# Optimization experiments

Hardware: AMD Instinct MI355X
Metric: run time of the kernel (lower is better)

## Reference

```python
import jax, jax.numpy as jnp
import numpy as np

NUM_HEADS = 12


def setup_inputs() -> dict:
    key = jax.random.key(0)
    ks = jax.random.split(key, 20)
    T, B, D = 1024, 8, 768
    s = 1.0 / np.sqrt(D)
    inp = {
        "query": jax.random.normal(ks[0], (T, B, D), jnp.float32),
        "key": jax.random.normal(ks[1], (T, B, D), jnp.float32),
        "value": jax.random.normal(ks[2], (T, B, D), jnp.float32),
        "ls_len": 512,
    }
    names = ["Wq", "Wk", "Wv", "Wqm", "Wkm", "Wvm", "Wo"]
    for i, n in enumerate(names):
        inp[n] = jax.random.normal(ks[3 + i], (D, D), jnp.float32) * s
        inp["b" + n[1:]] = jnp.zeros((D,), jnp.float32)
    return inp


def reference(query, key, value, ls_len, Wq, bq, Wk, bk, Wv, bv,
              Wqm, bqm, Wkm, bkm, Wvm, bvm, Wo, bo):
    T, B, D = query.shape
    H = NUM_HEADS
    hd = D // H
    scaling = float(hd) ** -0.5

    def proj(x, W, b):
        return x @ W.T + b

    # modal-split projections along the sequence (dim 0), then re-concat
    q = jnp.concatenate([proj(query[:ls_len], Wq, bq),
                         proj(query[ls_len:], Wqm, bqm)], axis=0) * scaling
    k = jnp.concatenate([proj(key[:ls_len], Wk, bk),
                         proj(key[ls_len:], Wkm, bkm)], axis=0)
    v = jnp.concatenate([proj(value[:ls_len], Wv, bv),
                         proj(value[ls_len:], Wvm, bvm)], axis=0)

    # (T, B, D) -> (B*H, T, hd)
    def to_heads(x):
        return x.reshape(x.shape[0], B * H, hd).transpose(1, 0, 2)

    q, k, v = to_heads(q), to_heads(k), to_heads(v)
    scores = jnp.einsum("bth,bsh->bts", q, k)        # (B*H, T, S)
    attn = jax.nn.softmax(scores, axis=-1)
    out = jnp.einsum("bts,bsh->bth", attn, v)        # (B*H, T, hd)
    out = out.transpose(1, 0, 2).reshape(T, B, D)
    return out @ Wo.T + bo
```

## Files before the change

kernel.cpp:

```cpp
#include <hip/hip_runtime.h>

#define T_  1024
#define B_  8
#define D_  768
#define H_  12
#define HD_ 64
#define BH_ 96
#define M_  8192
#define XSZ 6291456ull
#define WSZ 589824ull

typedef __attribute__((ext_vector_type(8))) short short8;
typedef __attribute__((ext_vector_type(4))) float f32x4;

__device__ __forceinline__ unsigned short f2bf(float f) {
    unsigned int u = __float_as_uint(f);
    u += 0x7FFF + ((u >> 16) & 1);
    return (unsigned short)(u >> 16);
}

__device__ __forceinline__ void g2lds16(const unsigned short* g, unsigned short* l) {
    __builtin_amdgcn_global_load_lds(
        (const __attribute__((address_space(1))) unsigned int*)(g),
        (__attribute__((address_space(3))) unsigned int*)(l),
        16, 0, 0);
}

__global__ __launch_bounds__(256)
void convert_kernel(const float* __restrict__ q, const float* __restrict__ k,
                    const float* __restrict__ v,
                    const float* __restrict__ wq, const float* __restrict__ wk,
                    const float* __restrict__ wv, const float* __restrict__ wqm,
                    const float* __restrict__ wkm, const float* __restrict__ wvm,
                    const float* __restrict__ wo,
                    unsigned short* __restrict__ dst)
{
    const int seg = blockIdx.y;
    const float* s; size_t off, n;
    switch (seg) {
        case 0: s = q;   off = 0;               n = XSZ; break;
        case 1: s = k;   off = XSZ;             n = XSZ; break;
        case 2: s = v;   off = 2*XSZ;           n = XSZ; break;
        case 3: s = wq;  off = 3*XSZ;           n = WSZ; break;
        case 4: s = wk;  off = 3*XSZ +   WSZ;   n = WSZ; break;
        case 5: s = wv;  off = 3*XSZ + 2*WSZ;   n = WSZ; break;
        case 6: s = wqm; off = 3*XSZ + 3*WSZ;   n = WSZ; break;
        case 7: s = wkm; off = 3*XSZ + 4*WSZ;   n = WSZ; break;
        case 8: s = wvm; off = 3*XSZ + 5*WSZ;   n = WSZ; break;
        default:s = wo;  off = 3*XSZ + 6*WSZ;   n = WSZ; break;
    }
    unsigned short* d = dst + off;
    const size_t stride = (size_t)gridDim.x * blockDim.x;
    for (size_t i = (size_t)blockIdx.x * blockDim.x + threadIdx.x; i < n / 4; i += stride) {
        const float4 f = reinterpret_cast<const float4*>(s)[i];
        ushort4 o;
        o.x = f2bf(f.x); o.y = f2bf(f.y); o.z = f2bf(f.z); o.w = f2bf(f.w);
        reinterpret_cast<ushort4*>(d)[i] = o;
    }
}

__device__ __forceinline__ void stage_tile32(const unsigned short* __restrict__ A,
                                             const unsigned short* __restrict__ B,
                                             int m0, int n0, int ks,
                                             unsigned short* lds, int buf, int tid)
{
    const int w = tid >> 6, l = tid & 63;
    const int rsub = l >> 2;
    const int cg   = (l & 3) ^ ((l >> 3) & 3);
    const int koff = ks * 32 + cg * 8;
    #pragma unroll
    for (int p = 0; p < 2; ++p) {
        const int rbase = p * 64 + w * 16;
        const int row   = rbase + rsub;
        g2lds16(&A[(size_t)(m0 + row) * D_ + koff],
                &lds[buf * 8192 + rbase * 32]);
        g2lds16(&B[(size_t)(n0 + row) * D_ + koff],
                &lds[buf * 8192 + 4096 + rbase * 32]);
    }
}

__device__ __forceinline__ void mfma_step32(const unsigned short* lds, int buf,
                                            int wr, int wc, int lr, int lg,
                                            f32x4 acc[4][4])
{
    const int slot = (lg ^ ((lr >> 1) & 3)) * 8;
    short8 a[4], b[4];
    #pragma unroll
    for (int m = 0; m < 4; ++m)
        a[m] = *reinterpret_cast<const short8*>(
            &lds[buf * 8192 + (wr * 64 + 16 * m + lr) * 32 + slot]);
    #pragma unroll
    for (int n = 0; n < 4; ++n)
        b[n] = *reinterpret_cast<const short8*>(
            &lds[buf * 8192 + 4096 + (wc * 64 + 16 * n + lr) * 32 + slot]);
    #pragma unroll
    for (int m = 0; m < 4; ++m)
        #pragma unroll
        for (int n = 0; n < 4; ++n)
            acc[m][n] = __builtin_amdgcn_mfma_f32_16x16x32_bf16(a[m], b[n], acc[m][n], 0, 0, 0);
}

#define GEMM_CORE(Aptr, Bptr)                                                  \
    f32x4 acc[4][4];                                                           \
    _Pragma("unroll") for (int m = 0; m < 4; ++m)                              \
        _Pragma("unroll") for (int n = 0; n < 4; ++n)                          \
            acc[m][n] = (f32x4){0.f, 0.f, 0.f, 0.f};                           \
    stage_tile32(Aptr, Bptr, m0, n0, 0, lds, 0, tid);                          \
    asm volatile("s_waitcnt vmcnt(0)" ::: "memory");                           \
    __builtin_amdgcn_s_barrier();                                              \
    for (int ks = 0; ks < 24; ++ks) {                                          \
        __builtin_amdgcn_sched_barrier(0);                                     \
        if (ks < 23) stage_tile32(Aptr, Bptr, m0, n0, ks + 1, lds, (ks + 1) & 1, tid); \
        mfma_step32(lds, ks & 1, wr, wc, lr, lg, acc);                         \
        asm volatile("s_waitcnt vmcnt(0) lgkmcnt(0)" ::: "memory");            \
        __builtin_amdgcn_sched_barrier(0);                                     \
        __builtin_amdgcn_s_barrier();                                          \
        __builtin_amdgcn_sched_barrier(0);                                     \
    }

__global__ __launch_bounds__(256)
void qkv_gemm(const unsigned short* __restrict__ xb,
              const unsigned short* __restrict__ wb,
              const int* __restrict__ ls_ptr,
              const float* __restrict__ bq,  const float* __restrict__ bk,
              const float* __restrict__ bv,  const float* __restrict__ bqm,
              const float* __restrict__ bkm, const float* __restrict__ bvm,
              unsigned short* __restrict__ qh, unsigned short* __restrict__ kh,
              unsigned short* __restrict__ vt)
{
    __shared__ unsigned short lds[16384];
    const int bid = blockIdx.x;
    const int L   = (bid & 7) * 144 + (bid >> 3);
    const int z   = L / 384;
    const int rem = L - z * 384;
    const int mi  = rem / 6;
    const int ni  = rem - mi * 6;
    const int m0 = mi * 128, n0 = ni * 128;

    const int tid = threadIdx.x;
    const int w = tid >> 6, l = tid & 63, lr = l & 15, lg = l >> 4;
    const int wr = w >> 1, wc = w & 1;

    const bool modal = (m0 >= ls_ptr[0] * B_);
    const unsigned short* A = xb + (size_t)z * XSZ;
    const unsigned short* W = wb + (size_t)(z + (modal ? 3 : 0)) * WSZ;
    const float* bias = modal ? (z == 0 ? bqm : z == 1 ? bkm : bvm)
                              : (z == 0 ? bq  : z == 1 ? bk  : bv);

    GEMM_CORE(A, W)

    float bn[4];
    #pragma unroll
    for (int n = 0; n < 4; ++n) bn[n] = bias[n0 + wc * 64 + 16 * n + lr];

    if (z < 2) {
        unsigned short* dst = (z == 0) ? qh : kh;
        const float scale = (z == 0) ? 0.18033688011112042f : 1.0f;
        #pragma unroll
        for (int m = 0; m < 4; ++m) {
            const int grb = m0 + wr * 64 + 16 * m + 4 * lg;
            #pragma unroll
            for (int n = 0; n < 4; ++n) {
                const int gc = n0 + wc * 64 + 16 * n + lr;
                const int h = gc >> 6, e = gc & 63;
                #pragma unroll
                for (int j = 0; j < 4; ++j) {
                    const int gr = grb + j, t = gr >> 3, b = gr & 7;
                    dst[((size_t)(b * H_ + h) * T_ + t) * HD_ + e] =
                        f2bf((acc[m][n][j] + bn[n]) * scale);
                }
            }
        }
    } else {
        #pragma unroll
        for (int m = 0; m < 4; ++m) {
            const int grb = m0 + wr * 64 + 16 * m + 4 * lg;
            #pragma unroll
            for (int n = 0; n < 4; ++n) {
                const int gc = n0 + wc * 64 + 16 * n + lr;
                const int h = gc >> 6, e = gc & 63;
                #pragma unroll
                for (int j = 0; j < 4; ++j) {
                    const int gr = grb + j, t = gr >> 3, b = gr & 7;
                    vt[((size_t)(b * H_ + h) * HD_ + e) * T_ + t] =
                        f2bf(acc[m][n][j] + bn[n]);
                }
            }
        }
    }
}

__global__ __launch_bounds__(256)
void out_gemm(const unsigned short* __restrict__ aob,
              const unsigned short* __restrict__ wo,
              const float* __restrict__ bo, float* __restrict__ out)
{
    __shared__ unsigned short lds[16384];
    const int bid = blockIdx.x;
    const int L   = (bid & 7) * 48 + (bid >> 3);
    const int mi  = L / 6, ni = L - mi * 6;
    const int m0 = mi * 128, n0 = ni * 128;

    const int tid = threadIdx.x;
    const int w = tid >> 6, l = tid & 63, lr = l & 15, lg = l >> 4;
    const int wr = w >> 1, wc = w & 1;

    GEMM_CORE(aob, wo)

    float bn[4];
    #pragma unroll
    for (int n = 0; n < 4; ++n) bn[n] = bo[n0 + wc * 64 + 16 * n + lr];

    #pragma unroll
    for (int m = 0; m < 4; ++m) {
        const int grb = m0 + wr * 64 + 16 * m + 4 * lg;
        #pragma unroll
        for (int n = 0; n < 4; ++n) {
            const int gc = n0 + wc * 64 + 16 * n + lr;
            #pragma unroll
            for (int j = 0; j < 4; ++j) {
                const int gr = grb + j;
                out[(size_t)gr * D_ + gc] = acc[m][n][j] + bn[n];
            }
        }
    }
}

__device__ __forceinline__ void stage_kv(const unsigned short* __restrict__ khh,
                                         const unsigned short* __restrict__ vth,
                                         int kt, unsigned short* KsB,
                                         unsigned short* VtB, int w, int l)
{
    const int rbase = w * 8;
    const int row   = rbase + (l >> 3);
    const int cg    = (l & 7) ^ ((l >> 3) & 7);
    g2lds16(&khh[(size_t)(kt * 64 + row) * HD_ + cg * 8], &KsB[rbase * 64]);
    g2lds16(&vth[(size_t)row * T_ + kt * 64 + cg * 8],    &VtB[rbase * 64]);
}

__global__ __launch_bounds__(512)
void attn_kernel_bf16(const unsigned short* __restrict__ qh,
                      const unsigned short* __restrict__ kh,
                      const unsigned short* __restrict__ vt,
                      unsigned short* __restrict__ aob)
{
    const int bid = blockIdx.x;
    const int L   = (bid & 7) * 96 + (bid >> 3);
    const int bh  = L >> 3;
    const int qt  = L & 7;

    const int tid = threadIdx.x;
    const int w   = tid >> 6;
    const int l   = tid & 63;
    const int lr  = l & 15;
    const int lg  = l >> 4;

    __shared__ unsigned short Ks[2][4096];
    __shared__ unsigned short Vt[2][4096];
    __shared__ unsigned short Ps[8192];

    const unsigned short* khh = kh + (size_t)bh * T_ * HD_;
    const unsigned short* vth = vt + (size_t)bh * HD_ * T_;
    const size_t qk_head = (size_t)bh * T_ * HD_;

    short8 qf[2];
    #pragma unroll
    for (int c = 0; c < 2; ++c)
        qf[c] = *reinterpret_cast<const short8*>(
            &qh[qk_head + (size_t)(qt * 128 + 16 * w + lr) * HD_ + 8 * lg + 32 * c]);

    const short one_bf = (short)0x3F80;
    const short8 ones8 = {one_bf, one_bf, one_bf, one_bf,
                          one_bf, one_bf, one_bf, one_bf};

    f32x4 o[4];
    #pragma unroll
    for (int ef = 0; ef < 4; ++ef) o[ef] = (f32x4){0.f, 0.f, 0.f, 0.f};
    f32x4 lsumf = (f32x4){0.f, 0.f, 0.f, 0.f};

    stage_kv(khh, vth, 0, Ks[0], Vt[0], w, l);
    asm volatile("s_waitcnt vmcnt(0)" ::: "memory");
    __builtin_amdgcn_s_barrier();

    int buf = 0;
    for (int kt = 0; kt < 16; ++kt) {
        __builtin_amdgcn_sched_barrier(0);
        if (kt < 15)
            stage_kv(khh, vth, kt + 1, Ks[buf ^ 1], Vt[buf ^ 1], w, l);

        f32x4 s[4];
        #pragma unroll
        for (int nf = 0; nf < 4; ++nf) s[nf] = (f32x4){0.f, 0.f, 0.f, 0.f};
        #pragma unroll
        for (int c = 0; c < 2; ++c) {
            #pragma unroll
            for (int nf = 0; nf < 4; ++nf) {
                const short8 kb = *reinterpret_cast<const short8*>(
                    &Ks[buf][(16 * nf + lr) * 64 + ((8 * lg + 32 * c) ^ ((lr & 7) << 3))]);
                s[nf] = __builtin_amdgcn_mfma_f32_16x16x32_bf16(qf[c], kb, s[nf], 0, 0, 0);
            }
        }

        #pragma unroll
        for (int r = 0; r < 4; ++r) {
            const int q  = 16 * w + 4 * lg + r;
            const int qx = ((4 * lg + r) & 7) << 3;
            #pragma unroll
            for (int nf = 0; nf < 4; ++nf)
                Ps[q * 64 + ((16 * nf + lr) ^ qx)] =
                    f2bf(exp2f(s[nf][r] - 16.0f));
        }
        asm volatile("s_waitcnt lgkmcnt(0)" ::: "memory");
        __builtin_amdgcn_sched_barrier(0);
        __builtin_amdgcn_s_barrier();
        __builtin_amdgcn_sched_barrier(0);

        const int prow = 16 * w + lr;
        #pragma unroll
        for (int c = 0; c < 2; ++c) {
            const short8 pa = *reinterpret_cast<const short8*>(
                &Ps[prow * 64 + ((8 * lg + 32 * c) ^ ((prow & 7) << 3))]);
            #pragma unroll
            for (int ef = 0; ef < 4; ++ef) {
                const short8 vb = *reinterpret_cast<const short8*>(
                    &Vt[buf][(16 * ef + lr) * 64 + ((8 * lg + 32 * c) ^ ((lr & 7) << 3))]);
                o[ef] = __builtin_amdgcn_mfma_f32_16x16x32_bf16(pa, vb, o[ef], 0, 0, 0);
            }
            lsumf = __builtin_amdgcn_mfma_f32_16x16x32_bf16(pa, ones8, lsumf, 0, 0, 0);
        }

        asm volatile("s_waitcnt vmcnt(0) lgkmcnt(0)" ::: "memory");
        __builtin_amdgcn_sched_barrier(0);
        __builtin_amdgcn_s_barrier();
        __builtin_amdgcn_sched_barrier(0);
        buf ^= 1;
    }

    const int b = bh / H_, h = bh % H_;
    #pragma unroll
    for (int r = 0; r < 4; ++r) {
        const int t = qt * 128 + 16 * w + 4 * lg + r;
        const float inv = 1.0f / lsumf[r];
        #pragma unroll
        for (int ef = 0; ef < 4; ++ef)
            aob[((size_t)t * B_ + b) * D_ + h * HD_ + 16 * ef + lr] =
                f2bf(o[ef][r] * inv);
    }
}

extern "C" void kernel_launch(void* const* d_in, const int* in_sizes, int n_in,
                              void* d_out, int out_size, void* d_ws, size_t ws_size,
                              hipStream_t stream)
{
    const float* query = (const float*)d_in[0];
    const float* keyi  = (const float*)d_in[1];
    const float* value = (const float*)d_in[2];
    const int*   lsp   = (const int*)  d_in[3];
    const float* Wq  = (const float*)d_in[4],  *bq  = (const float*)d_in[5];
    const float* Wk  = (const float*)d_in[6],  *bk  = (const float*)d_in[7];
    const float* Wv  = (const float*)d_in[8],  *bv  = (const float*)d_in[9];
    const float* Wqm = (const float*)d_in[10], *bqm = (const float*)d_in[11];
    const float* Wkm = (const float*)d_in[12], *bkm = (const float*)d_in[13];
    const float* Wvm = (const float*)d_in[14], *bvm = (const float*)d_in[15];
    const float* Wo  = (const float*)d_in[16], *bo  = (const float*)d_in[17];

    unsigned short* ws = (unsigned short*)d_ws;
    unsigned short* xb  = ws;
    unsigned short* wb  = xb + 3 * XSZ;
    unsigned short* qh  = wb + 7 * WSZ;
    unsigned short* kh  = qh + XSZ;
    unsigned short* vt  = kh + XSZ;
    unsigned short* aob = vt + XSZ;

    dim3 gc_(512, 10);
    convert_kernel<<<gc_, 256, 0, stream>>>(query, keyi, value,
                                            Wq, Wk, Wv, Wqm, Wkm, Wvm, Wo, xb);

    qkv_gemm<<<1152, 256, 0, stream>>>(xb, wb, lsp, bq, bk, bv, bqm, bkm, bvm,
                                       qh, kh, vt);

    attn_kernel_bf16<<<768, 512, 0, stream>>>(qh, kh, vt, aob);

    out_gemm<<<384, 256, 0, stream>>>(aob, wb + 6 * WSZ, bo, (float*)d_out);
}
```

Baseline: 187.4 us.

## Fuse fp32-to-bf16 activation conversion into QKV GEMM and triple-buffer out GEMM

```diff
diff --git a/kernel.cpp b/kernel.cpp
--- a/kernel.cpp
+++ b/kernel.cpp
@@ -27,31 +27,26 @@
 }
 
 __global__ __launch_bounds__(256)
-void convert_kernel(const float* __restrict__ q, const float* __restrict__ k,
-                    const float* __restrict__ v,
-                    const float* __restrict__ wq, const float* __restrict__ wk,
-                    const float* __restrict__ wv, const float* __restrict__ wqm,
-                    const float* __restrict__ wkm, const float* __restrict__ wvm,
-                    const float* __restrict__ wo,
-                    unsigned short* __restrict__ dst)
+void convert_w_kernel(const float* __restrict__ wq, const float* __restrict__ wk,
+                      const float* __restrict__ wv, const float* __restrict__ wqm,
+                      const float* __restrict__ wkm, const float* __restrict__ wvm,
+                      const float* __restrict__ wo,
+                      unsigned short* __restrict__ dst)
 {
     const int seg = blockIdx.y;
-    const float* s; size_t off, n;
+    const float* s;
     switch (seg) {
-        case 0: s = q;   off = 0;               n = XSZ; break;
-        case 1: s = k;   off = XSZ;             n = XSZ; break;
-        case 2: s = v;   off = 2*XSZ;           n = XSZ; break;
-        case 3: s = wq;  off = 3*XSZ;           n = WSZ; break;
-        case 4: s = wk;  off = 3*XSZ +   WSZ;   n = WSZ; break;
-        case 5: s = wv;  off = 3*XSZ + 2*WSZ;   n = WSZ; break;
-        case 6: s = wqm; off = 3*XSZ + 3*WSZ;   n = WSZ; break;
-        case 7: s = wkm; off = 3*XSZ + 4*WSZ;   n = WSZ; break;
-        case 8: s = wvm; off = 3*XSZ + 5*WSZ;   n = WSZ; break;
-        default:s = wo;  off = 3*XSZ + 6*WSZ;   n = WSZ; break;
-    }
-    unsigned short* d = dst + off;
+        case 0: s = wq;  break;
+        case 1: s = wk;  break;
+        case 2: s = wv;  break;
+        case 3: s = wqm; break;
+        case 4: s = wkm; break;
+        case 5: s = wvm; break;
+        default:s = wo;  break;
+    }
+    unsigned short* d = dst + (size_t)seg * WSZ;
     const size_t stride = (size_t)gridDim.x * blockDim.x;
-    for (size_t i = (size_t)blockIdx.x * blockDim.x + threadIdx.x; i < n / 4; i += stride) {
+    for (size_t i = (size_t)blockIdx.x * blockDim.x + threadIdx.x; i < WSZ / 4; i += stride) {
         const float4 f = reinterpret_cast<const float4*>(s)[i];
         ushort4 o;
         o.x = f2bf(f.x); o.y = f2bf(f.y); o.z = f2bf(f.z); o.w = f2bf(f.w);
@@ -59,26 +54,6 @@
     }
 }
 
-__device__ __forceinline__ void stage_tile32(const unsigned short* __restrict__ A,
-                                             const unsigned short* __restrict__ B,
-                                             int m0, int n0, int ks,
-                                             unsigned short* lds, int buf, int tid)
-{
-    const int w = tid >> 6, l = tid & 63;
-    const int rsub = l >> 2;
-    const int cg   = (l & 3) ^ ((l >> 3) & 3);
-    const int koff = ks * 32 + cg * 8;
-    #pragma unroll
-    for (int p = 0; p < 2; ++p) {
-        const int rbase = p * 64 + w * 16;
-        const int row   = rbase + rsub;
-        g2lds16(&A[(size_t)(m0 + row) * D_ + koff],
-                &lds[buf * 8192 + rbase * 32]);
-        g2lds16(&B[(size_t)(n0 + row) * D_ + koff],
-                &lds[buf * 8192 + 4096 + rbase * 32]);
-    }
-}
-
 __device__ __forceinline__ void mfma_step32(const unsigned short* lds, int buf,
                                             int wr, int wc, int lr, int lg,
                                             f32x4 acc[4][4])
@@ -100,26 +75,10 @@
             acc[m][n] = __builtin_amdgcn_mfma_f32_16x16x32_bf16(a[m], b[n], acc[m][n], 0, 0, 0);
 }
 
-#define GEMM_CORE(Aptr, Bptr)                                                  \
-    f32x4 acc[4][4];                                                           \
-    _Pragma("unroll") for (int m = 0; m < 4; ++m)                              \
-        _Pragma("unroll") for (int n = 0; n < 4; ++n)                          \
-            acc[m][n] = (f32x4){0.f, 0.f, 0.f, 0.f};                           \
-    stage_tile32(Aptr, Bptr, m0, n0, 0, lds, 0, tid);                          \
-    asm volatile("s_waitcnt vmcnt(0)" ::: "memory");                           \
-    __builtin_amdgcn_s_barrier();                                              \
-    for (int ks = 0; ks < 24; ++ks) {                                          \
-        __builtin_amdgcn_sched_barrier(0);                                     \
-        if (ks < 23) stage_tile32(Aptr, Bptr, m0, n0, ks + 1, lds, (ks + 1) & 1, tid); \
-        mfma_step32(lds, ks & 1, wr, wc, lr, lg, acc);                         \
-        asm volatile("s_waitcnt vmcnt(0) lgkmcnt(0)" ::: "memory");            \
-        __builtin_amdgcn_sched_barrier(0);                                     \
-        __builtin_amdgcn_s_barrier();                                          \
-        __builtin_amdgcn_sched_barrier(0);                                     \
-    }
-
 __global__ __launch_bounds__(256)
-void qkv_gemm(const unsigned short* __restrict__ xb,
+void qkv_gemm(const float* __restrict__ query,
+              const float* __restrict__ keyi,
+              const float* __restrict__ value,
               const unsigned short* __restrict__ wb,
               const int* __restrict__ ls_ptr,
               const float* __restrict__ bq,  const float* __restrict__ bk,
@@ -142,12 +101,76 @@
     const int wr = w >> 1, wc = w & 1;
 
     const bool modal = (m0 >= ls_ptr[0] * B_);
-    const unsigned short* A = xb + (size_t)z * XSZ;
+    const float* A32 = (z == 0) ? query : (z == 1) ? keyi : value;
     const unsigned short* W = wb + (size_t)(z + (modal ? 3 : 0)) * WSZ;
     const float* bias = modal ? (z == 0 ? bqm : z == 1 ? bkm : bvm)
                               : (z == 0 ? bq  : z == 1 ? bk  : bv);
 
-    GEMM_CORE(A, W)
+    const int arow_s = tid >> 2;
+    const int ac     = tid & 3;
+    const int aslot  = (ac ^ ((tid >> 3) & 3)) * 8;
+
+    float4 ax[2][2];
+
+#define LOADX(ks)                                                              \
+    _Pragma("unroll") for (int p = 0; p < 2; ++p) {                            \
+        const float* src = &A32[(size_t)(m0 + p * 64 + arow_s) * D_ +          \
+                                (ks) * 32 + ac * 8];                           \
+        ax[p][0] = *reinterpret_cast<const float4*>(src);                      \
+        ax[p][1] = *reinterpret_cast<const float4*>(src + 4);                  \
+    }
+
+#define WRITEX(buf)                                                            \
+    _Pragma("unroll") for (int p = 0; p < 2; ++p) {                            \
+        unsigned short v8[8];                                                  \
+        v8[0] = f2bf(ax[p][0].x); v8[1] = f2bf(ax[p][0].y);                    \
+        v8[2] = f2bf(ax[p][0].z); v8[3] = f2bf(ax[p][0].w);                    \
+        v8[4] = f2bf(ax[p][1].x); v8[5] = f2bf(ax[p][1].y);                    \
+        v8[6] = f2bf(ax[p][1].z); v8[7] = f2bf(ax[p][1].w);                    \
+        *reinterpret_cast<short8*>(                                            \
+            &lds[(buf) * 8192 + (p * 64 + arow_s) * 32 + aslot]) =             \
+            *reinterpret_cast<const short8*>(v8);                              \
+    }
+
+#define STAGEB(ks, buf)                                                        \
+    {                                                                          \
+        const int rsub = l >> 2;                                               \
+        const int cg   = (l & 3) ^ ((l >> 3) & 3);                             \
+        const int koff = (ks) * 32 + cg * 8;                                   \
+        _Pragma("unroll") for (int p = 0; p < 2; ++p) {                        \
+            const int rbase = p * 64 + w * 16;                                 \
+            g2lds16(&W[(size_t)(n0 + rbase + rsub) * D_ + koff],               \
+                    &lds[(buf) * 8192 + 4096 + rbase * 32]);                   \
+        }                                                                      \
+    }
+
+    f32x4 acc[4][4];
+    #pragma unroll
+    for (int m = 0; m < 4; ++m)
+        #pragma unroll
+        for (int n = 0; n < 4; ++n)
+            acc[m][n] = (f32x4){0.f, 0.f, 0.f, 0.f};
+
+    LOADX(0)
+    STAGEB(0, 0)
+    WRITEX(0)
+    __syncthreads();
+
+    int buf = 0;
+    for (int ks = 0; ks < 24; ++ks) {
+        if (ks < 23) {
+            LOADX(ks + 1)
+            STAGEB(ks + 1, buf ^ 1)
+        }
+        mfma_step32(lds, buf, wr, wc, lr, lg, acc);
+        if (ks < 23) { WRITEX(buf ^ 1) }
+        __syncthreads();
+        buf ^= 1;
+    }
+
+#undef LOADX
+#undef WRITEX
+#undef STAGEB
 
     float bn[4];
     #pragma unroll
@@ -190,12 +213,32 @@
     }
 }
 
+__device__ __forceinline__ void stage_tile32(const unsigned short* __restrict__ A,
+                                             const unsigned short* __restrict__ B,
+                                             int m0, int n0, int ks,
+                                             unsigned short* lds, int buf, int tid)
+{
+    const int w = tid >> 6, l = tid & 63;
+    const int rsub = l >> 2;
+    const int cg   = (l & 3) ^ ((l >> 3) & 3);
+    const int koff = ks * 32 + cg * 8;
+    #pragma unroll
+    for (int p = 0; p < 2; ++p) {
+        const int rbase = p * 64 + w * 16;
+        const int row   = rbase + rsub;
+        g2lds16(&A[(size_t)(m0 + row) * D_ + koff],
+                &lds[buf * 8192 + rbase * 32]);
+        g2lds16(&B[(size_t)(n0 + row) * D_ + koff],
+                &lds[buf * 8192 + 4096 + rbase * 32]);
+    }
+}
+
 __global__ __launch_bounds__(256)
 void out_gemm(const unsigned short* __restrict__ aob,
               const unsigned short* __restrict__ wo,
               const float* __restrict__ bo, float* __restrict__ out)
 {
-    __shared__ unsigned short lds[16384];
+    __shared__ unsigned short lds[24576];
     const int bid = blockIdx.x;
     const int L   = (bid & 7) * 48 + (bid >> 3);
     const int mi  = L / 6, ni = L - mi * 6;
@@ -205,7 +248,30 @@
     const int w = tid >> 6, l = tid & 63, lr = l & 15, lg = l >> 4;
     const int wr = w >> 1, wc = w & 1;
 
-    GEMM_CORE(aob, wo)
+    f32x4 acc[4][4];
+    #pragma unroll
+    for (int m = 0; m < 4; ++m)
+        #pragma unroll
+        for (int n = 0; n < 4; ++n)
+            acc[m][n] = (f32x4){0.f, 0.f, 0.f, 0.f};
+
+    stage_tile32(aob, wo, m0, n0, 0, lds, 0, tid);
+    stage_tile32(aob, wo, m0, n0, 1, lds, 1, tid);
+    stage_tile32(aob, wo, m0, n0, 2, lds, 2, tid);
+    for (int ks = 0; ks < 24; ++ks) {
+        if (ks < 22)       { asm volatile("s_waitcnt vmcnt(8) lgkmcnt(0)" ::: "memory"); }
+        else if (ks == 22) { asm volatile("s_waitcnt vmcnt(4) lgkmcnt(0)" ::: "memory"); }
+        else               { asm volatile("s_waitcnt vmcnt(0) lgkmcnt(0)" ::: "memory"); }
+        __builtin_amdgcn_sched_barrier(0);
+        __builtin_amdgcn_s_barrier();
+        __builtin_amdgcn_sched_barrier(0);
+        mfma_step32(lds, ks % 3, wr, wc, lr, lg, acc);
+        asm volatile("s_waitcnt lgkmcnt(0)" ::: "memory");
+        __builtin_amdgcn_sched_barrier(0);
+        __builtin_amdgcn_s_barrier();
+        __builtin_amdgcn_sched_barrier(0);
+        if (ks < 21) stage_tile32(aob, wo, m0, n0, ks + 3, lds, ks % 3, tid);
+    }
 
     float bn[4];
     #pragma unroll
@@ -365,18 +431,17 @@
     const float* Wo  = (const float*)d_in[16], *bo  = (const float*)d_in[17];
 
     unsigned short* ws = (unsigned short*)d_ws;
-    unsigned short* xb  = ws;
-    unsigned short* wb  = xb + 3 * XSZ;
+    unsigned short* wb  = ws;
     unsigned short* qh  = wb + 7 * WSZ;
     unsigned short* kh  = qh + XSZ;
     unsigned short* vt  = kh + XSZ;
     unsigned short* aob = vt + XSZ;
 
-    dim3 gc_(512, 10);
-    convert_kernel<<<gc_, 256, 0, stream>>>(query, keyi, value,
-                                            Wq, Wk, Wv, Wqm, Wkm, Wvm, Wo, xb);
-
-    qkv_gemm<<<1152, 256, 0, stream>>>(xb, wb, lsp, bq, bk, bv, bqm, bkm, bvm,
+    dim3 gcw(96, 7);
+    convert_w_kernel<<<gcw, 256, 0, stream>>>(Wq, Wk, Wv, Wqm, Wkm, Wvm, Wo, wb);
+
+    qkv_gemm<<<1152, 256, 0, stream>>>(query, keyi, value, wb, lsp,
+                                       bq, bk, bv, bqm, bkm, bvm,
                                        qh, kh, vt);
 
     attn_kernel_bf16<<<768, 512, 0, stream>>>(qh, kh, vt, aob);
```

Measured after the change: 180.1 us. 1.04x faster.

## Load QKV GEMM operands directly to registers; triple-buffer out-projection LDS pipeline

Applied to the files above, without the earlier changes.

```diff
diff --git a/kernel.cpp b/kernel.cpp
--- a/kernel.cpp
+++ b/kernel.cpp
@@ -59,65 +59,6 @@
     }
 }
 
-__device__ __forceinline__ void stage_tile32(const unsigned short* __restrict__ A,
-                                             const unsigned short* __restrict__ B,
-                                             int m0, int n0, int ks,
-                                             unsigned short* lds, int buf, int tid)
-{
-    const int w = tid >> 6, l = tid & 63;
-    const int rsub = l >> 2;
-    const int cg   = (l & 3) ^ ((l >> 3) & 3);
-    const int koff = ks * 32 + cg * 8;
-    #pragma unroll
-    for (int p = 0; p < 2; ++p) {
-        const int rbase = p * 64 + w * 16;
-        const int row   = rbase + rsub;
-        g2lds16(&A[(size_t)(m0 + row) * D_ + koff],
-                &lds[buf * 8192 + rbase * 32]);
-        g2lds16(&B[(size_t)(n0 + row) * D_ + koff],
-                &lds[buf * 8192 + 4096 + rbase * 32]);
-    }
-}
-
-__device__ __forceinline__ void mfma_step32(const unsigned short* lds, int buf,
-                                            int wr, int wc, int lr, int lg,
-                                            f32x4 acc[4][4])
-{
-    const int slot = (lg ^ ((lr >> 1) & 3)) * 8;
-    short8 a[4], b[4];
-    #pragma unroll
-    for (int m = 0; m < 4; ++m)
-        a[m] = *reinterpret_cast<const short8*>(
-            &lds[buf * 8192 + (wr * 64 + 16 * m + lr) * 32 + slot]);
-    #pragma unroll
-    for (int n = 0; n < 4; ++n)
-        b[n] = *reinterpret_cast<const short8*>(
-            &lds[buf * 8192 + 4096 + (wc * 64 + 16 * n + lr) * 32 + slot]);
-    #pragma unroll
-    for (int m = 0; m < 4; ++m)
-        #pragma unroll
-        for (int n = 0; n < 4; ++n)
-            acc[m][n] = __builtin_amdgcn_mfma_f32_16x16x32_bf16(a[m], b[n], acc[m][n], 0, 0, 0);
-}
-
-#define GEMM_CORE(Aptr, Bptr)                                                  \
-    f32x4 acc[4][4];                                                           \
-    _Pragma("unroll") for (int m = 0; m < 4; ++m)                              \
-        _Pragma("unroll") for (int n = 0; n < 4; ++n)                          \
-            acc[m][n] = (f32x4){0.f, 0.f, 0.f, 0.f};                           \
-    stage_tile32(Aptr, Bptr, m0, n0, 0, lds, 0, tid);                          \
-    asm volatile("s_waitcnt vmcnt(0)" ::: "memory");                           \
-    __builtin_amdgcn_s_barrier();                                              \
-    for (int ks = 0; ks < 24; ++ks) {                                          \
-        __builtin_amdgcn_sched_barrier(0);                                     \
-        if (ks < 23) stage_tile32(Aptr, Bptr, m0, n0, ks + 1, lds, (ks + 1) & 1, tid); \
-        mfma_step32(lds, ks & 1, wr, wc, lr, lg, acc);                         \
-        asm volatile("s_waitcnt vmcnt(0) lgkmcnt(0)" ::: "memory");            \
-        __builtin_amdgcn_sched_barrier(0);                                     \
-        __builtin_amdgcn_s_barrier();                                          \
-        __builtin_amdgcn_sched_barrier(0);                                     \
-    }
-
 __global__ __launch_bounds__(256)
 void qkv_gemm(const unsigned short* __restrict__ xb,
               const unsigned short* __restrict__ wb,
@@ -128,7 +69,6 @@
               unsigned short* __restrict__ qh, unsigned short* __restrict__ kh,
               unsigned short* __restrict__ vt)
 {
-    __shared__ unsigned short lds[16384];
     const int bid = blockIdx.x;
     const int L   = (bid & 7) * 144 + (bid >> 3);
     const int z   = L / 384;
@@ -147,7 +87,45 @@
     const float* bias = modal ? (z == 0 ? bqm : z == 1 ? bkm : bvm)
                               : (z == 0 ? bq  : z == 1 ? bk  : bv);
 
-    GEMM_CORE(A, W)
+    const unsigned short* arow[4];
+    const unsigned short* brow[4];
+    #pragma unroll
+    for (int m = 0; m < 4; ++m)
+        arow[m] = &A[(size_t)(m0 + wr * 64 + 16 * m + lr) * D_ + lg * 8];
+    #pragma unroll
+    for (int n = 0; n < 4; ++n)
+        brow[n] = &W[(size_t)(n0 + wc * 64 + 16 * n + lr) * D_ + lg * 8];
+
+    f32x4 acc[4][4];
+    #pragma unroll
+    for (int m = 0; m < 4; ++m)
+        #pragma unroll
+        for (int n = 0; n < 4; ++n)
+            acc[m][n] = (f32x4){0.f, 0.f, 0.f, 0.f};
+
+    short8 aE[4], bE[4], aO[4], bO[4];
+
+#define LOADF(aa, bb, ks)                                                      \
+    _Pragma("unroll") for (int m = 0; m < 4; ++m)                              \
+        aa[m] = *reinterpret_cast<const short8*>(arow[m] + (ks) * 32);         \
+    _Pragma("unroll") for (int n = 0; n < 4; ++n)                              \
+        bb[n] = *reinterpret_cast<const short8*>(brow[n] + (ks) * 32);
+
+#define MFMASET(aa, bb)                                                        \
+    _Pragma("unroll") for (int m = 0; m < 4; ++m)                              \
+        _Pragma("unroll") for (int n = 0; n < 4; ++n)                          \
+            acc[m][n] = __builtin_amdgcn_mfma_f32_16x16x32_bf16(aa[m], bb[n], acc[m][n], 0, 0, 0);
+
+    LOADF(aE, bE, 0)
+    #pragma unroll
+    for (int ks = 0; ks < 24; ks += 2) {
+        if (ks + 1 < 24) { LOADF(aO, bO, ks + 1) }
+        MFMASET(aE, bE)
+        if (ks + 2 < 24) { LOADF(aE, bE, ks + 2) }
+        if (ks + 1 < 24) { MFMASET(aO, bO) }
+    }
+#undef LOADF
+#undef MFMASET
 
     float bn[4];
     #pragma unroll
@@ -190,12 +168,53 @@
     }
 }
 
+__device__ __forceinline__ void stage_tile32(const unsigned short* __restrict__ A,
+                                             const unsigned short* __restrict__ B,
+                                             int m0, int n0, int ks,
+                                             unsigned short* lds, int buf, int tid)
+{
+    const int w = tid >> 6, l = tid & 63;
+    const int rsub = l >> 2;
+    const int cg   = (l & 3) ^ ((l >> 3) & 3);
+    const int koff = ks * 32 + cg * 8;
+    #pragma unroll
+    for (int p = 0; p < 2; ++p) {
+        const int rbase = p * 64 + w * 16;
+        const int row   = rbase + rsub;
+        g2lds16(&A[(size_t)(m0 + row) * D_ + koff],
+                &lds[buf * 8192 + rbase * 32]);
+        g2lds16(&B[(size_t)(n0 + row) * D_ + koff],
+                &lds[buf * 8192 + 4096 + rbase * 32]);
+    }
+}
+
+__device__ __forceinline__ void mfma_step32(const unsigned short* lds, int buf,
+                                            int wr, int wc, int lr, int lg,
+                                            f32x4 acc[4][4])
+{
+    const int slot = (lg ^ ((lr >> 1) & 3)) * 8;
+    short8 a[4], b[4];
+    #pragma unroll
+    for (int m = 0; m < 4; ++m)
+        a[m] = *reinterpret_cast<const short8*>(
+            &lds[buf * 8192 + (wr * 64 + 16 * m + lr) * 32 + slot]);
+    #pragma unroll
+    for (int n = 0; n < 4; ++n)
+        b[n] = *reinterpret_cast<const short8*>(
+            &lds[buf * 8192 + 4096 + (wc * 64 + 16 * n + lr) * 32 + slot]);
+    #pragma unroll
+    for (int m = 0; m < 4; ++m)
+        #pragma unroll
+        for (int n = 0; n < 4; ++n)
+            acc[m][n] = __builtin_amdgcn_mfma_f32_16x16x32_bf16(a[m], b[n], acc[m][n], 0, 0, 0);
+}
+
 __global__ __launch_bounds__(256)
 void out_gemm(const unsigned short* __restrict__ aob,
               const unsigned short* __restrict__ wo,
               const float* __restrict__ bo, float* __restrict__ out)
 {
-    __shared__ unsigned short lds[16384];
+    __shared__ unsigned short lds[24576];
     const int bid = blockIdx.x;
     const int L   = (bid & 7) * 48 + (bid >> 3);
     const int mi  = L / 6, ni = L - mi * 6;
@@ -205,7 +224,30 @@
     const int w = tid >> 6, l = tid & 63, lr = l & 15, lg = l >> 4;
     const int wr = w >> 1, wc = w & 1;
 
-    GEMM_CORE(aob, wo)
+    f32x4 acc[4][4];
+    #pragma unroll
+    for (int m = 0; m < 4; ++m)
+        #pragma unroll
+        for (int n = 0; n < 4; ++n)
+            acc[m][n] = (f32x4){0.f, 0.f, 0.f, 0.f};
+
+    stage_tile32(aob, wo, m0, n0, 0, lds, 0, tid);
+    stage_tile32(aob, wo, m0, n0, 1, lds, 1, tid);
+    stage_tile32(aob, wo, m0, n0, 2, lds, 2, tid);
+    for (int ks = 0; ks < 24; ++ks) {
+        if (ks < 22)       { asm volatile("s_waitcnt vmcnt(8) lgkmcnt(0)" ::: "memory"); }
+        else if (ks == 22) { asm volatile("s_waitcnt vmcnt(4) lgkmcnt(0)" ::: "memory"); }
+        else               { asm volatile("s_waitcnt vmcnt(0) lgkmcnt(0)" ::: "memory"); }
+        __builtin_amdgcn_sched_barrier(0);
+        __builtin_amdgcn_s_barrier();
+        __builtin_amdgcn_sched_barrier(0);
+        mfma_step32(lds, ks % 3, wr, wc, lr, lg, acc);
+        asm volatile("s_waitcnt lgkmcnt(0)" ::: "memory");
+        __builtin_amdgcn_sched_barrier(0);
+        __builtin_amdgcn_s_barrier();
+        __builtin_amdgcn_sched_barrier(0);
+        if (ks < 21) stage_tile32(aob, wo, m0, n0, ks + 3, lds, ks % 3, tid);
+    }
 
     float bn[4];
     #pragma unroll
```

Measured after the change: 236.4 us. 1.26x slower.
